# Kernel tuning notes

Hardware: AMD Instinct MI355X
Metric: run time of the kernel (lower is better)

The kernel has to match this reference:

```python
import jax, jax.numpy as jnp
import numpy as np


def setup_inputs() -> dict:
    key = jax.random.key(0)
    kq, kk, kv, km = jax.random.split(key, 4)
    B, H, S, D = 4, 16, 2048, 64
    query = jax.random.normal(kq, (B, H, S, D), dtype=jnp.float32)
    k = jax.random.normal(kk, (B, H, S, D), dtype=jnp.float32)
    value = jax.random.normal(kv, (B, H, S, D), dtype=jnp.float32)
    mask = jax.random.randint(km, (B, S, S), 0, 2, dtype=jnp.int32)
    return {"query": query, "key": k, "value": value, "mask": mask}


def reference(query, key, value, mask):
    # query/key/value: [B, H, S, D]; mask: [B, S, S] (0 = masked out)
    d = query.shape[-1]
    scale = 1.0 / jnp.sqrt(jnp.asarray(d, dtype=query.dtype))
    scores = jnp.einsum('bhqd,bhkd->bhqk', query, key) * scale
    m = (mask[:, None, :, :] == 0)  # broadcast over heads, matches mask.unsqueeze(1).eq(0)
    min_value = jnp.finfo(scores.dtype).min
    scores = jnp.where(m, min_value, scores)
    attn = jax.nn.softmax(scores, axis=-1)
    attn = jnp.where(m, jnp.asarray(0.0, attn.dtype), attn)
    out = jnp.einsum('bhqk,bhkd->bhqd', attn, value)
    return (out, attn)
```

## Files before the change

kernel.cpp:

```cpp
#include <hip/hip_runtime.h>
#include <hip/hip_bf16.h>


typedef __attribute__((ext_vector_type(8))) short bf16x8;
typedef __attribute__((ext_vector_type(4))) float f32x4;
typedef __attribute__((ext_vector_type(4))) int i32x4;
typedef __attribute__((ext_vector_type(2))) unsigned int u32x2;

#define MFMA16(A, B, C) __builtin_amdgcn_mfma_f32_16x16x32_bf16((A), (B), (C), 0, 0, 0)

constexpr int Bsz = 4, Hsz = 16, Ssz = 2048, Dsz = 64;
constexpr int KBLK = 64;
constexpr int NT   = Ssz / KBLK;
constexpr float SCALE = 0.125f;

static __device__ __forceinline__ short f2bf(float f) {
  __hip_bfloat16 h = __float2bfloat16(f);
  return __builtin_bit_cast(short, h);
}

static __device__ __forceinline__ void wg_barrier() {
  __builtin_amdgcn_sched_barrier(0);
  asm volatile("s_waitcnt lgkmcnt(0)" ::: "memory");
  __builtin_amdgcn_sched_barrier(0);
  __builtin_amdgcn_s_barrier();
  __builtin_amdgcn_sched_barrier(0);
}

__global__ __launch_bounds__(512, 8)
void attn_denom(const float* __restrict__ Qg, const float* __restrict__ Kg,
                const int* __restrict__ Mg, float* __restrict__ wsL,
                unsigned short* __restrict__ wsM)
{
  __shared__ short sK[2][KBLK][72];

  const int qt = blockIdx.x, bh = blockIdx.y;
  const int q0 = qt * 128;
  const int tid = threadIdx.x, lane = tid & 63, w = tid >> 6;
  const int lr = lane & 15, lg = lane >> 4;

  const size_t bhSD = (size_t)bh * (Ssz * Dsz);
  const float* Qb = Qg + bhSD;
  const float* Kb = Kg + bhSD;
  const int b = bh >> 4;
  const int qrow = q0 + w * 16 + lr;
  const int* Mrow = Mg + ((size_t)b * Ssz + qrow) * Ssz;
  unsigned short* wsMq = wsM + (size_t)(b * Ssz + qrow) * (NT * 4) + lg;

  bf16x8 qf[2];
  {
    const float* qp = Qb + (size_t)qrow * Dsz + lg * 8;
#pragma unroll
    for (int h = 0; h < 2; ++h) {
      f32x4 a = *(const f32x4*)(qp + h * 32);
      f32x4 c2 = *(const f32x4*)(qp + h * 32 + 4);
      bf16x8 t;
#pragma unroll
      for (int j = 0; j < 4; ++j) { t[j] = f2bf(a[j] * SCALE); t[4 + j] = f2bf(c2[j] * SCALE); }
      qf[h] = t;
    }
  }

  const int krow = tid >> 3, kd0 = (tid & 7) * 8;
  {
    const float* kp = Kb + (size_t)krow * Dsz + kd0;
    f32x4 a = *(const f32x4*)kp, c2 = *(const f32x4*)(kp + 4);
    bf16x8 t;
#pragma unroll
    for (int j = 0; j < 4; ++j) { t[j] = f2bf(a[j]); t[4 + j] = f2bf(c2[j]); }
    *(bf16x8*)(&sK[0][krow][kd0]) = t;
  }
  wg_barrier();

  float lacc = 0.f;
  for (int t = 0; t < NT; ++t) {
    const int cur = t & 1;
    f32x4 ka = {0.f,0.f,0.f,0.f}, kb2 = {0.f,0.f,0.f,0.f};
    if (t + 1 < NT) {
      const float* kp = Kb + (size_t)((t + 1) * KBLK + krow) * Dsz + kd0;
      ka  = *(const f32x4*)kp;
      kb2 = *(const f32x4*)(kp + 4);
    }
    unsigned bits = 0;
#pragma unroll
    for (int cb = 0; cb < 4; ++cb) {
      const short* kr = &sK[cur][cb * 16 + lr][0];
      bf16x8 a0 = *(const bf16x8*)(kr + lg * 8);
      bf16x8 a1 = *(const bf16x8*)(kr + 32 + lg * 8);
      f32x4 c = {0.f, 0.f, 0.f, 0.f};
      c = MFMA16(a0, qf[0], c);
      c = MFMA16(a1, qf[1], c);
      i32x4 mv = *(const i32x4*)(Mrow + t * KBLK + cb * 16 + lg * 4);
#pragma unroll
      for (int r = 0; r < 4; ++r) {
        lacc += mv[r] ? __expf(c[r]) : 0.f;
        bits |= (mv[r] ? 1u : 0u) << (cb * 4 + r);
      }
    }
    wsMq[t * 4] = (unsigned short)bits;
    if (t + 1 < NT) {
      bf16x8 t2;
#pragma unroll
      for (int j = 0; j < 4; ++j) { t2[j] = f2bf(ka[j]); t2[4 + j] = f2bf(kb2[j]); }
      *(bf16x8*)(&sK[cur ^ 1][krow][kd0]) = t2;
    }
    wg_barrier();
  }

  lacc += __shfl_xor(lacc, 16, 64);
  lacc += __shfl_xor(lacc, 32, 64);
  if (lane < 16)
    wsL[(size_t)bh * Ssz + qrow] = (lacc > 0.f) ? 1.f / lacc : 0.f;
}

__global__ __launch_bounds__(512, 6)
void attn_emit(const float* __restrict__ Qg, const float* __restrict__ Kg,
               const float* __restrict__ Vg, const float* __restrict__ wsL,
               const unsigned short* __restrict__ wsM,
               float* __restrict__ Og, float* __restrict__ Ag)
{
  __shared__ __align__(16) char smem[5 * 64 * 72 * 2];
  auto sK  = (short(*)[KBLK][72])(smem);
  auto sVt = (short(*)[Dsz][72])(smem + 2 * 9216);
  auto sP  = (short(*)[72])(smem + 4 * 9216);
  auto sO  = (float(*)[68])(smem);

  const int qt = blockIdx.x, bh = blockIdx.y;
  const int q0 = qt * 64;
  const int tid = threadIdx.x, lane = tid & 63, wid = tid >> 6;
  const int wq = wid >> 1, wk = wid & 1;
  const int lr = lane & 15, lg = lane >> 4;

  const size_t bhSD = (size_t)bh * (Ssz * Dsz);
  const float* Qb = Qg + bhSD;
  const float* Kb = Kg + bhSD;
  const float* Vb = Vg + bhSD;
  const int b = bh >> 4;
  float* Ob = Og + bhSD;
  float* Ab = Ag + (size_t)bh * ((size_t)Ssz * Ssz);

  const int qrow = q0 + wq * 16 + lr;
  float* Arow = Ab + (size_t)qrow * Ssz;
  const float invl = wsL[(size_t)bh * Ssz + qrow];
  const unsigned short* wsMq = wsM + (size_t)(b * Ssz + qrow) * (NT * 4) + lg;
  const int mshift = wk * 8;

  bf16x8 qf[2];
  {
    const float* qp = Qb + (size_t)qrow * Dsz + lg * 8;
#pragma unroll
    for (int h = 0; h < 2; ++h) {
      f32x4 a = *(const f32x4*)(qp + h * 32);
      f32x4 c2 = *(const f32x4*)(qp + h * 32 + 4);
      bf16x8 t;
#pragma unroll
      for (int j = 0; j < 4; ++j) { t[j] = f2bf(a[j] * SCALE); t[4 + j] = f2bf(c2[j] * SCALE); }
      qf[h] = t;
    }
  }

  const int krow = tid >> 3;
  const int kd0  = (tid & 7) * 8;
  const int vkv  = tid & 63;
  const int vd0  = (tid >> 6) * 8;
  const int kb0  = wk * 32 + lg * 4;

  f32x4 oacc[4] = {{0,0,0,0},{0,0,0,0},{0,0,0,0},{0,0,0,0}};

  {
    const float* kp = Kb + (size_t)krow * Dsz + kd0;
    f32x4 a = *(const f32x4*)kp, c2 = *(const f32x4*)(kp + 4);
    bf16x8 t;
#pragma unroll
    for (int j = 0; j < 4; ++j) { t[j] = f2bf(a[j]); t[4 + j] = f2bf(c2[j]); }
    *(bf16x8*)(&sK[0][krow][kd0]) = t;

    const float* vp = Vb + (size_t)vkv * Dsz + vd0;
    f32x4 va = *(const f32x4*)vp, vb = *(const f32x4*)(vp + 4);
#pragma unroll
    for (int j = 0; j < 4; ++j) {
      sVt[0][vd0 + j][vkv]     = f2bf(va[j]);
      sVt[0][vd0 + 4 + j][vkv] = f2bf(vb[j]);
    }
  }
  unsigned mbn = wsMq[0];
  wg_barrier();

  for (int t = 0; t < NT; ++t) {
    const int cur = t & 1;
    const unsigned mb = mbn;
    f32x4 ka = {0.f,0.f,0.f,0.f}, kb2 = {0.f,0.f,0.f,0.f};
    f32x4 va = {0.f,0.f,0.f,0.f}, vb2 = {0.f,0.f,0.f,0.f};
    if (t + 1 < NT) {
      const float* kp = Kb + (size_t)((t + 1) * KBLK + krow) * Dsz + kd0;
      ka  = *(const f32x4*)kp;
      kb2 = *(const f32x4*)(kp + 4);
      const float* vp = Vb + (size_t)((t + 1) * KBLK + vkv) * Dsz + vd0;
      va  = *(const f32x4*)vp;
      vb2 = *(const f32x4*)(vp + 4);
      mbn = wsMq[(t + 1) * 4];
    }
    __builtin_amdgcn_s_setprio(1);
#pragma unroll
    for (int cb = 0; cb < 2; ++cb) {
      const short* kr = &sK[cur][wk * 32 + cb * 16 + lr][0];
      bf16x8 a0 = *(const bf16x8*)(kr + lg * 8);
      bf16x8 a1 = *(const bf16x8*)(kr + 32 + lg * 8);
      f32x4 c = {0.f, 0.f, 0.f, 0.f};
      c = MFMA16(a0, qf[0], c);
      c = MFMA16(a1, qf[1], c);
      f32x4 p;
#pragma unroll
      for (int r = 0; r < 4; ++r)
        p[r] = ((mb >> (mshift + cb * 4 + r)) & 1u) ? __expf(c[r]) * invl : 0.f;
      __builtin_nontemporal_store(p, (f32x4*)(Arow + t * KBLK + kb0 + cb * 16));
      unsigned plo = (unsigned short)f2bf(p[0]) | ((unsigned)(unsigned short)f2bf(p[1]) << 16);
      unsigned phi = (unsigned short)f2bf(p[2]) | ((unsigned)(unsigned short)f2bf(p[3]) << 16);
      u32x2 wv = {plo, phi};
      *(u32x2*)(&sP[wq * 16 + lr][wk * 32 + cb * 16 + lg * 4]) = wv;
    }
    bf16x8 pa = *(const bf16x8*)(&sP[wq * 16 + lr][wk * 32 + lg * 8]);
#pragma unroll
    for (int nb = 0; nb < 4; ++nb) {
      bf16x8 vb = *(const bf16x8*)(&sVt[cur][nb * 16 + lr][wk * 32 + lg * 8]);
      oacc[nb] = MFMA16(pa, vb, oacc[nb]);
    }
    __builtin_amdgcn_s_setprio(0);
    if (t + 1 < NT) {
      bf16x8 t2;
#pragma unroll
      for (int j = 0; j < 4; ++j) { t2[j] = f2bf(ka[j]); t2[4 + j] = f2bf(kb2[j]); }
      *(bf16x8*)(&sK[cur ^ 1][krow][kd0]) = t2;
#pragma unroll
      for (int j = 0; j < 4; ++j) {
        sVt[cur ^ 1][vd0 + j][vkv]     = f2bf(va[j]);
        sVt[cur ^ 1][vd0 + 4 + j][vkv] = f2bf(vb2[j]);
      }
    }
    wg_barrier();
  }

  if (wk == 0) {
#pragma unroll
    for (int nb = 0; nb < 4; ++nb)
#pragma unroll
      for (int r = 0; r < 4; ++r)
        sO[wq * 16 + lg * 4 + r][nb * 16 + lr] = oacc[nb][r];
  }
  wg_barrier();
  if (wk == 1) {
#pragma unroll
    for (int nb = 0; nb < 4; ++nb)
#pragma unroll
      for (int r = 0; r < 4; ++r) {
        float v = sO[wq * 16 + lg * 4 + r][nb * 16 + lr] + oacc[nb][r];
        __builtin_nontemporal_store(v, Ob + (size_t)(q0 + wq * 16 + lg * 4 + r) * Dsz + nb * 16 + lr);
      }
  }
}

extern "C" void kernel_launch(void* const* d_in, const int* in_sizes, int n_in,
                              void* d_out, int out_size, void* d_ws, size_t ws_size,
                              hipStream_t stream) {
  const float* Q = (const float*)d_in[0];
  const float* K = (const float*)d_in[1];
  const float* V = (const float*)d_in[2];
  const int*   M = (const int*)d_in[3];
  float* Out  = (float*)d_out;
  float* Attn = Out + (size_t)Bsz * Hsz * Ssz * Dsz;
  float* wsL = (float*)d_ws;
  unsigned short* wsM = (unsigned short*)((char*)d_ws + (size_t)Bsz * Hsz * Ssz * sizeof(float));
  attn_denom<<<dim3(Ssz / 128, Bsz * Hsz), 512, 0, stream>>>(Q, K, M, wsL, wsM);
  attn_emit <<<dim3(Ssz / 64,  Bsz * Hsz), 512, 0, stream>>>(Q, K, V, wsL, wsM, Out, Attn);
}
```

Measured before the change: 504.8 us.

## Feed P to PV MFMA from registers instead of LDS staging

Drops the shared-memory P tile. Each 16x16 score block, converted to bf16, is fed directly as the A operand of 16x16x16 bf16 MFMAs, written as inline asm, against matching slices of V^T. This removes an LDS write/read round trip and shrinks LDS so occupancy can rise to 8 waves/SIMD via launch bounds. In exchange it issues twice as many smaller MFMAs and relies on hand-placed s_nop hazards in inline asm.

```diff
diff --git a/kernel.cpp b/kernel.cpp
--- a/kernel.cpp
+++ b/kernel.cpp
@@ -3,11 +3,11 @@
 
 
 typedef __attribute__((ext_vector_type(8))) short bf16x8;
+typedef __attribute__((ext_vector_type(4))) short bf16x4;
 typedef __attribute__((ext_vector_type(4))) float f32x4;
 typedef __attribute__((ext_vector_type(4))) int i32x4;
-typedef __attribute__((ext_vector_type(2))) unsigned int u32x2;
-
-#define MFMA16(A, B, C) __builtin_amdgcn_mfma_f32_16x16x32_bf16((A), (B), (C), 0, 0, 0)
+
+#define MFMA32(A, B, C) __builtin_amdgcn_mfma_f32_16x16x32_bf16((A), (B), (C), 0, 0, 0)
 
 constexpr int Bsz = 4, Hsz = 16, Ssz = 2048, Dsz = 64;
 constexpr int KBLK = 64;
@@ -88,8 +88,8 @@
       bf16x8 a0 = *(const bf16x8*)(kr + lg * 8);
       bf16x8 a1 = *(const bf16x8*)(kr + 32 + lg * 8);
       f32x4 c = {0.f, 0.f, 0.f, 0.f};
-      c = MFMA16(a0, qf[0], c);
-      c = MFMA16(a1, qf[1], c);
+      c = MFMA32(a0, qf[0], c);
+      c = MFMA32(a1, qf[1], c);
       i32x4 mv = *(const i32x4*)(Mrow + t * KBLK + cb * 16 + lg * 4);
 #pragma unroll
       for (int r = 0; r < 4; ++r) {
@@ -113,16 +113,15 @@
     wsL[(size_t)bh * Ssz + qrow] = (lacc > 0.f) ? 1.f / lacc : 0.f;
 }
 
-__global__ __launch_bounds__(512, 6)
+__global__ __launch_bounds__(512, 8)
 void attn_emit(const float* __restrict__ Qg, const float* __restrict__ Kg,
                const float* __restrict__ Vg, const float* __restrict__ wsL,
                const unsigned short* __restrict__ wsM,
                float* __restrict__ Og, float* __restrict__ Ag)
 {
-  __shared__ __align__(16) char smem[5 * 64 * 72 * 2];
+  __shared__ __align__(16) char smem[4 * 64 * 72 * 2];
   auto sK  = (short(*)[KBLK][72])(smem);
   auto sVt = (short(*)[Dsz][72])(smem + 2 * 9216);
-  auto sP  = (short(*)[72])(smem + 4 * 9216);
   auto sO  = (float(*)[68])(smem);
 
   const int qt = blockIdx.x, bh = blockIdx.y;
@@ -198,7 +197,7 @@
       const float* vp = Vb + (size_t)((t + 1) * KBLK + vkv) * Dsz + vd0;
       va  = *(const f32x4*)vp;
       vb2 = *(const f32x4*)(vp + 4);
-      mbn = wsMq[(t + 1) * 4];
+      mbn  = wsMq[(t + 1) * 4];
     }
     __builtin_amdgcn_s_setprio(1);
 #pragma unroll
@@ -207,23 +206,27 @@
       bf16x8 a0 = *(const bf16x8*)(kr + lg * 8);
       bf16x8 a1 = *(const bf16x8*)(kr + 32 + lg * 8);
       f32x4 c = {0.f, 0.f, 0.f, 0.f};
-      c = MFMA16(a0, qf[0], c);
-      c = MFMA16(a1, qf[1], c);
+      c = MFMA32(a0, qf[0], c);
+      c = MFMA32(a1, qf[1], c);
       f32x4 p;
 #pragma unroll
       for (int r = 0; r < 4; ++r)
         p[r] = ((mb >> (mshift + cb * 4 + r)) & 1u) ? __expf(c[r]) * invl : 0.f;
       __builtin_nontemporal_store(p, (f32x4*)(Arow + t * KBLK + kb0 + cb * 16));
-      unsigned plo = (unsigned short)f2bf(p[0]) | ((unsigned)(unsigned short)f2bf(p[1]) << 16);
-      unsigned phi = (unsigned short)f2bf(p[2]) | ((unsigned)(unsigned short)f2bf(p[3]) << 16);
-      u32x2 wv = {plo, phi};
-      *(u32x2*)(&sP[wq * 16 + lr][wk * 32 + cb * 16 + lg * 4]) = wv;
-    }
-    bf16x8 pa = *(const bf16x8*)(&sP[wq * 16 + lr][wk * 32 + lg * 8]);
-#pragma unroll
-    for (int nb = 0; nb < 4; ++nb) {
-      bf16x8 vb = *(const bf16x8*)(&sVt[cur][nb * 16 + lr][wk * 32 + lg * 8]);
-      oacc[nb] = MFMA16(pa, vb, oacc[nb]);
+      bf16x4 pf = {f2bf(p[0]), f2bf(p[1]), f2bf(p[2]), f2bf(p[3])};
+      bf16x4 vf0 = *(const bf16x4*)(&sVt[cur][0 * 16 + lr][wk * 32 + cb * 16 + lg * 4]);
+      bf16x4 vf1 = *(const bf16x4*)(&sVt[cur][1 * 16 + lr][wk * 32 + cb * 16 + lg * 4]);
+      bf16x4 vf2 = *(const bf16x4*)(&sVt[cur][2 * 16 + lr][wk * 32 + cb * 16 + lg * 4]);
+      bf16x4 vf3 = *(const bf16x4*)(&sVt[cur][3 * 16 + lr][wk * 32 + cb * 16 + lg * 4]);
+      asm volatile(
+        "s_nop 1\n\t"
+        "v_mfma_f32_16x16x16_bf16 %0, %4, %5, %0\n\t"
+        "v_mfma_f32_16x16x16_bf16 %1, %4, %6, %1\n\t"
+        "v_mfma_f32_16x16x16_bf16 %2, %4, %7, %2\n\t"
+        "v_mfma_f32_16x16x16_bf16 %3, %4, %8, %3\n\t"
+        "s_nop 2"
+        : "+v"(oacc[0]), "+v"(oacc[1]), "+v"(oacc[2]), "+v"(oacc[3])
+        : "v"(pf), "v"(vf0), "v"(vf1), "v"(vf2), "v"(vf3));
     }
     __builtin_amdgcn_s_setprio(0);
     if (t + 1 < NT) {
@@ -239,6 +242,8 @@
     }
     wg_barrier();
   }
+
+  asm volatile("s_nop 7\n\ts_nop 7" :::);
 
   if (wk == 0) {
 #pragma unroll
```

Result: slower. 873.0 us (+72.9%).
